# Kernel tuning notes

Measured on AMD Instinct MI355X. Metric: run time of the kernel, lower is better.

## Reference

```python
import jax, jax.numpy as jnp
import numpy as np

K_MAX = 3
ITERS = 3
NEG_BIG = -1e9


def squash(x):
    # x: [..., O]
    sn = jnp.sum(jnp.square(x), axis=-1, keepdims=True)
    factor = sn / (1.0 + sn) / jnp.sqrt(sn + 1e-8)
    return factor * x


def setup_inputs() -> dict:
    key = jax.random.key(0)
    k1, k2, k3, k4 = jax.random.split(key, 4)
    N, L, D, O = 4096, 200, 64, 64
    behavior_embs = jax.random.normal(k1, (N, L, D), dtype=jnp.float32)
    W = jax.random.normal(k2, (D, O), dtype=jnp.float32)  # init_std=1.0
    routing_logits_init = jax.random.normal(k3, (N, K_MAX, L), dtype=jnp.float32)
    seq_len = jax.random.randint(k4, (N, 1), 0, L, dtype=jnp.int32)
    return {
        "behavior_embs": behavior_embs,
        "W": W,
        "routing_logits_init": routing_logits_init,
        "seq_len": seq_len,
    }


def reference(behavior_embs, W, routing_logits_init, seq_len):
    N, L, D = behavior_embs.shape
    # mask: [N, K_MAX, L] -- valid positions along L, tiled across capsules
    mask = jnp.arange(L)[None, None, :] < seq_len[:, None, :]  # [N,1,L]
    mask = jnp.broadcast_to(mask, (N, K_MAX, L))

    mappings = jnp.matmul(behavior_embs, W)          # [N, L, O]
    m_det = jax.lax.stop_gradient(mappings)         # routing uses detached mappings

    logits = routing_logits_init                     # [N, K_MAX, L]
    for _ in range(ITERS - 1):
        padded = jnp.where(mask, logits, NEG_BIG)
        # NOTE: softmax over the capsule dim (axis=1), as in the original
        weights = jax.nn.softmax(padded, axis=1)     # [N, K_MAX, L]
        candidates = jnp.matmul(weights, m_det)      # [N, K_MAX, O]
        interests = squash(candidates)
        logits = logits + jnp.einsum('nko,nlo->nkl', interests, m_det)

    padded = jnp.where(mask, logits, NEG_BIG)
    weights = jax.nn.softmax(padded, axis=1)
    candidates = jnp.matmul(weights, mappings)       # final iter uses non-detached
    interests = squash(candidates)                   # [N, K_MAX, O]
    return interests
```

## Files before the change

kernel.cpp:

```cpp
#include <hip/hip_runtime.h>
#include <math.h>

typedef _Float16 f16;
typedef _Float16 f16x8 __attribute__((ext_vector_type(8)));
typedef float f32x4 __attribute__((ext_vector_type(4)));

#define LSEQ 200
#define LT 13
#define NCHUNK 1664
#define EBUF (NCHUNK*8)
#define SPB 4

__global__ __launch_bounds__(256, 2)
void capsule_kernel(const float* __restrict__ E,
                    const float* __restrict__ W,
                    const float* __restrict__ RL,
                    const int* __restrict__ SL,
                    float* __restrict__ out,
                    int Ntot)
{
    __shared__ __attribute__((aligned(16))) f16 e_sw[2*EBUF];
    __shared__ __attribute__((aligned(16))) f16 w_p[3*224];
    __shared__ __attribute__((aligned(16))) f16 i_c[3*80];
    __shared__ __attribute__((aligned(16))) f16 iw_c[3*72];
    __shared__ __attribute__((aligned(16))) float cand[192];

    const int n0 = blockIdx.x * SPB;
    const int t = threadIdx.x;
    const int lane = t & 63;
    const int wv = t >> 6;
    const int q = lane >> 4;
    const int cc = lane & 15;
    const int cmin = cc < 3 ? cc : 2;
    const int o_own = wv*16 + cc;

    f16x8 wB0, wB1, wt0, wt1;
    {
        f16x8 h;
        #pragma unroll
        for (int j = 0; j < 8; j++) h[j] = (f16)W[(q*8 + j)*64 + o_own];
        wB0 = h;
        #pragma unroll
        for (int j = 0; j < 8; j++) h[j] = (f16)W[(32 + q*8 + j)*64 + o_own];
        wB1 = h;
        const float4 a0 = *(const float4*)(W + o_own*64 + q*8);
        const float4 b0 = *(const float4*)(W + o_own*64 + q*8 + 4);
        f16x8 g0 = { (f16)a0.x,(f16)a0.y,(f16)a0.z,(f16)a0.w,
                     (f16)b0.x,(f16)b0.y,(f16)b0.z,(f16)b0.w };
        wt0 = g0;
        const float4 a1 = *(const float4*)(W + o_own*64 + 32 + q*8);
        const float4 b1 = *(const float4*)(W + o_own*64 + 32 + q*8 + 4);
        f16x8 g1 = { (f16)a1.x,(f16)a1.y,(f16)a1.z,(f16)a1.w,
                     (f16)b1.x,(f16)b1.y,(f16)b1.z,(f16)b1.w };
        wt1 = g1;
    }

    if (t < 12) {
        const f16x8 hz = {(f16)0.f,(f16)0.f,(f16)0.f,(f16)0.f,
                          (f16)0.f,(f16)0.f,(f16)0.f,(f16)0.f};
        *(f16x8*)&w_p[(t>>2)*224 + 192 + (t&3)*8] = hz;
    }

    const float4 f4z = make_float4(0.f, 0.f, 0.f, 0.f);
    float4 va[7], vb[7];

#define STAGE_ISSUE(NN)                                                       \
    {                                                                         \
        const float* Eb_ = E + (size_t)(NN) * (LSEQ*64);                      \
        _Pragma("unroll")                                                     \
        for (int i = 0; i < 7; i++) {                                         \
            int g = t + i*256;                                                \
            va[i] = f4z; vb[i] = f4z;                                         \
            if (g < NCHUNK) {                                                 \
                int l = (g >> 7)*16 + (g & 15);                               \
                int kb = ((g >> 6) & 1)*32 + ((g >> 4) & 3)*8;                \
                if (l < LSEQ) {                                               \
                    va[i] = *(const float4*)(Eb_ + l*64 + kb);                \
                    vb[i] = *(const float4*)(Eb_ + l*64 + kb + 4);            \
                }                                                             \
            }                                                                 \
        }                                                                     \
    }

#define STAGE_COMMIT(BASE)                                                    \
    {                                                                         \
        _Pragma("unroll")                                                     \
        for (int i = 0; i < 7; i++) {                                         \
            int g = t + i*256;                                                \
            if (g < NCHUNK) {                                                 \
                f16x8 h = { (f16)va[i].x,(f16)va[i].y,(f16)va[i].z,(f16)va[i].w,\
                            (f16)vb[i].x,(f16)vb[i].y,(f16)vb[i].z,(f16)vb[i].w };\
                *(f16x8*)&e_sw[(BASE) + g*8] = h;                             \
            }                                                                 \
        }                                                                     \
    }

    if (n0 < Ntot) {
        STAGE_ISSUE(n0)
        STAGE_COMMIT(0)
    }

    for (int j = 0; j < SPB; ++j) {
        const int nn = n0 + j;
        if (nn >= Ntot) break;
        const int cur = (j & 1) * EBUF;
        const int nxt = ((j + 1) & 1) * EBUF;
        const bool pf = (j + 1 < SPB) && (nn + 1 < Ntot);

        __syncthreads();

        float lg[4][3];
        #pragma unroll
        for (int slot = 0; slot < 4; slot++) {
            int Tn = wv + slot*4;
            if (Tn < LT && lane < 16) {
                int l = Tn*16 + lane;
                if (l < LSEQ) {
                    lg[slot][0] = RL[(size_t)nn*600 + l];
                    lg[slot][1] = RL[(size_t)nn*600 + 200 + l];
                    lg[slot][2] = RL[(size_t)nn*600 + 400 + l];
                }
            }
        }
        const int s = SL[nn];

        if (pf) STAGE_ISSUE(nn + 1)

        f16x8 mc0, mc1, mc2, mc3, mc4, mc5, mc6;

#define MM_PAIR(P, MC)                                                        \
        {                                                                     \
            f32x4 c0 = {0.f, 0.f, 0.f, 0.f};                                  \
            f32x4 c1 = {0.f, 0.f, 0.f, 0.f};                                  \
            f16x8 a00 = *(f16x8*)&e_sw[cur + (((2*(P)  )*2 + 0)*64 + lane)*8];\
            c0 = __builtin_amdgcn_mfma_f32_16x16x32_f16(a00, wB0, c0, 0,0,0); \
            f16x8 a01 = *(f16x8*)&e_sw[cur + (((2*(P)  )*2 + 1)*64 + lane)*8];\
            c0 = __builtin_amdgcn_mfma_f32_16x16x32_f16(a01, wB1, c0, 0,0,0); \
            f16x8 a10 = *(f16x8*)&e_sw[cur + (((2*(P)+1)*2 + 0)*64 + lane)*8];\
            c1 = __builtin_amdgcn_mfma_f32_16x16x32_f16(a10, wB0, c1, 0,0,0); \
            f16x8 a11 = *(f16x8*)&e_sw[cur + (((2*(P)+1)*2 + 1)*64 + lane)*8];\
            c1 = __builtin_amdgcn_mfma_f32_16x16x32_f16(a11, wB1, c1, 0,0,0); \
            f16x8 hh;                                                         \
            hh[0]=(f16)c0[0]; hh[1]=(f16)c0[1]; hh[2]=(f16)c0[2]; hh[3]=(f16)c0[3];\
            hh[4]=(f16)c1[0]; hh[5]=(f16)c1[1]; hh[6]=(f16)c1[2]; hh[7]=(f16)c1[3];\
            MC = hh;                                                          \
        }

        MM_PAIR(0, mc0)
        MM_PAIR(1, mc1)
        MM_PAIR(2, mc2)
        MM_PAIR(3, mc3)
        MM_PAIR(4, mc4)
        MM_PAIR(5, mc5)
#undef MM_PAIR
        {
            f32x4 c0 = {0.f, 0.f, 0.f, 0.f};
            f16x8 a00 = *(f16x8*)&e_sw[cur + ((12*2 + 0)*64 + lane)*8];
            c0 = __builtin_amdgcn_mfma_f32_16x16x32_f16(a00, wB0, c0, 0,0,0);
            f16x8 a01 = *(f16x8*)&e_sw[cur + ((12*2 + 1)*64 + lane)*8];
            c0 = __builtin_amdgcn_mfma_f32_16x16x32_f16(a01, wB1, c0, 0,0,0);
            f16x8 hh;
            hh[0]=(f16)c0[0]; hh[1]=(f16)c0[1]; hh[2]=(f16)c0[2]; hh[3]=(f16)c0[3];
            hh[4]=(f16)0.f;   hh[5]=(f16)0.f;   hh[6]=(f16)0.f;   hh[7]=(f16)0.f;
            mc6 = hh;
        }

        if (pf) STAGE_COMMIT(nxt)

        #pragma unroll
        for (int slot = 0; slot < 4; slot++) {
            int Tn = wv + slot*4;
            if (Tn < LT && lane < 16) {
                int l = Tn*16 + lane;
                if (l < LSEQ) {
                    float w0, w1, w2;
                    if (l < s) {
                        float l0 = lg[slot][0], l1 = lg[slot][1], l2 = lg[slot][2];
                        float mx = fmaxf(fmaxf(l0, l1), l2);
                        float e0 = expf(l0 - mx), e1 = expf(l1 - mx), e2 = expf(l2 - mx);
                        float inv = 1.f / (e0 + e1 + e2);
                        w0 = e0*inv; w1 = e1*inv; w2 = e2*inv;
                    } else {
                        w0 = w1 = w2 = (1.f/3.f);
                    }
                    int wbase = (l>>5)*32 + (((l>>2)&3)<<3) + (((l>>4)&1)<<2) + (l&3);
                    w_p[wbase]       = (f16)w0;
                    w_p[224 + wbase] = (f16)w1;
                    w_p[448 + wbase] = (f16)w2;
                }
            }
        }
        __syncthreads();

        for (int iter = 0; iter < 3; iter++) {
            f32x4 ca = {0.f, 0.f, 0.f, 0.f};
#define CAND_STEP(P, MC)                                                      \
            { f16x8 a = *(f16x8*)&w_p[cmin*224 + (P)*32 + q*8];               \
              ca = __builtin_amdgcn_mfma_f32_16x16x32_f16(a, MC, ca, 0,0,0); }
            CAND_STEP(0, mc0)
            CAND_STEP(1, mc1)
            CAND_STEP(2, mc2)
            CAND_STEP(3, mc3)
            CAND_STEP(4, mc4)
            CAND_STEP(5, mc5)
            CAND_STEP(6, mc6)
#undef CAND_STEP
            if (q == 0) {
                cand[0*64 + o_own] = ca[0];
                cand[1*64 + o_own] = ca[1];
                cand[2*64 + o_own] = ca[2];
            }
            __syncthreads();

            if (t < 192) {
                float x = cand[t];
                float sq = x*x;
                #pragma unroll
                for (int off = 32; off >= 1; off >>= 1) sq += __shfl_xor(sq, off, 64);
                float factor = sq / ((1.f + sq) * sqrtf(sq + 1e-8f));
                float y = factor * x;
                if (iter < 2) {
                    i_c[(t >> 6)*80 + (t & 63)] = (f16)y;
                } else {
                    out[(size_t)nn*192 + t] = y;
                }
            }
            if (iter == 2) break;
            __syncthreads();

            {
                f16x8 ia0 = *(f16x8*)&i_c[cmin*80 + q*8];
                f16x8 ia1 = *(f16x8*)&i_c[cmin*80 + 32 + q*8];
                f32x4 dw = {0.f, 0.f, 0.f, 0.f};
                dw = __builtin_amdgcn_mfma_f32_16x16x32_f16(ia0, wt0, dw, 0,0,0);
                dw = __builtin_amdgcn_mfma_f32_16x16x32_f16(ia1, wt1, dw, 0,0,0);
                if (q == 0) {
                    iw_c[0*72 + o_own] = (f16)dw[0];
                    iw_c[1*72 + o_own] = (f16)dw[1];
                    iw_c[2*72 + o_own] = (f16)dw[2];
                }
            }
            __syncthreads();

            f16x8 iwa0 = *(f16x8*)&iw_c[cmin*72 + q*8];
            f16x8 iwa1 = *(f16x8*)&iw_c[cmin*72 + 32 + q*8];
            #pragma unroll
            for (int slot = 0; slot < 4; slot++) {
                int Tn = wv + slot*4;
                if (Tn < LT) {
                    f32x4 da = {0.f, 0.f, 0.f, 0.f};
                    f16x8 b0 = *(f16x8*)&e_sw[cur + ((Tn*2 + 0)*64 + lane)*8];
                    da = __builtin_amdgcn_mfma_f32_16x16x32_f16(iwa0, b0, da, 0,0,0);
                    f16x8 b1 = *(f16x8*)&e_sw[cur + ((Tn*2 + 1)*64 + lane)*8];
                    da = __builtin_amdgcn_mfma_f32_16x16x32_f16(iwa1, b1, da, 0,0,0);
                    if (lane < 16) {
                        int l = Tn*16 + lane;
                        if (l < LSEQ) {
                            float w0, w1, w2;
                            if (l < s) {
                                float l0 = lg[slot][0] + da[0];
                                float l1 = lg[slot][1] + da[1];
                                float l2 = lg[slot][2] + da[2];
                                lg[slot][0] = l0; lg[slot][1] = l1; lg[slot][2] = l2;
                                float mx = fmaxf(fmaxf(l0, l1), l2);
                                float e0 = expf(l0 - mx), e1 = expf(l1 - mx), e2 = expf(l2 - mx);
                                float inv = 1.f / (e0 + e1 + e2);
                                w0 = e0*inv; w1 = e1*inv; w2 = e2*inv;
                            } else {
                                w0 = w1 = w2 = (1.f/3.f);
                            }
                            int wbase = (l>>5)*32 + (((l>>2)&3)<<3) + (((l>>4)&1)<<2) + (l&3);
                            w_p[wbase]       = (f16)w0;
                            w_p[224 + wbase] = (f16)w1;
                            w_p[448 + wbase] = (f16)w2;
                        }
                    }
                }
            }
            __syncthreads();
        }
    }
#undef STAGE_ISSUE
#undef STAGE_COMMIT
}

extern "C" void kernel_launch(void* const* d_in, const int* in_sizes, int n_in,
                              void* d_out, int out_size, void* d_ws, size_t ws_size,
                              hipStream_t stream) {
    const float* E  = (const float*)d_in[0];
    const float* W  = (const float*)d_in[1];
    const float* RL = (const float*)d_in[2];
    const int*   SL = (const int*)d_in[3];
    float* o = (float*)d_out;
    const int N = in_sizes[3];
    const int NB = (N + SPB - 1) / SPB;
    capsule_kernel<<<dim3(NB), dim3(256), 0, stream>>>(E, W, RL, SL, o, N);
}
```

Measured before the change: 311.1 us.

## Single-buffer embedding tile and raise occupancy, prefetching during routing iterations

Replaces the double-buffered fp16 embedding tile in shared memory with a single buffer, halving LDS per block, and raises the launch-bounds target from 2 to 4 blocks per CU. The prefetch of the next sample's embeddings is now issued at routing iteration 1 and written to LDS at iteration 2, once the current tile is no longer read. This trades explicit double-buffer overlap for more resident blocks to hide latency. The tighter register budget must still hold the 56 prefetch floats, which risks spills. The overlap window is also shorter.

```diff
diff --git a/kernel.cpp b/kernel.cpp
--- a/kernel.cpp
+++ b/kernel.cpp
@@ -8,10 +8,9 @@
 #define LSEQ 200
 #define LT 13
 #define NCHUNK 1664
-#define EBUF (NCHUNK*8)
 #define SPB 4
 
-__global__ __launch_bounds__(256, 2)
+__global__ __launch_bounds__(256, 4)
 void capsule_kernel(const float* __restrict__ E,
                     const float* __restrict__ W,
                     const float* __restrict__ RL,
@@ -19,7 +18,7 @@
                     float* __restrict__ out,
                     int Ntot)
 {
-    __shared__ __attribute__((aligned(16))) f16 e_sw[2*EBUF];
+    __shared__ __attribute__((aligned(16))) f16 e_sw[NCHUNK*8];
     __shared__ __attribute__((aligned(16))) f16 w_p[3*224];
     __shared__ __attribute__((aligned(16))) f16 i_c[3*80];
     __shared__ __attribute__((aligned(16))) f16 iw_c[3*72];
@@ -82,7 +81,7 @@
         }                                                                     \
     }
 
-#define STAGE_COMMIT(BASE)                                                    \
+#define STAGE_COMMIT()                                                        \
     {                                                                         \
         _Pragma("unroll")                                                     \
         for (int i = 0; i < 7; i++) {                                         \
@@ -90,24 +89,20 @@
             if (g < NCHUNK) {                                                 \
                 f16x8 h = { (f16)va[i].x,(f16)va[i].y,(f16)va[i].z,(f16)va[i].w,\
                             (f16)vb[i].x,(f16)vb[i].y,(f16)vb[i].z,(f16)vb[i].w };\
-                *(f16x8*)&e_sw[(BASE) + g*8] = h;                             \
+                *(f16x8*)&e_sw[g*8] = h;                                      \
             }                                                                 \
         }                                                                     \
     }
 
     if (n0 < Ntot) {
         STAGE_ISSUE(n0)
-        STAGE_COMMIT(0)
+        STAGE_COMMIT()
     }
 
     for (int j = 0; j < SPB; ++j) {
         const int nn = n0 + j;
         if (nn >= Ntot) break;
-        const int cur = (j & 1) * EBUF;
-        const int nxt = ((j + 1) & 1) * EBUF;
         const bool pf = (j + 1 < SPB) && (nn + 1 < Ntot);
-
-        __syncthreads();
 
         float lg[4][3];
         #pragma unroll
@@ -124,7 +119,7 @@
         }
         const int s = SL[nn];
 
-        if (pf) STAGE_ISSUE(nn + 1)
+        __syncthreads();
 
         f16x8 mc0, mc1, mc2, mc3, mc4, mc5, mc6;
 
@@ -132,13 +127,13 @@
         {                                                                     \
             f32x4 c0 = {0.f, 0.f, 0.f, 0.f};                                  \
             f32x4 c1 = {0.f, 0.f, 0.f, 0.f};                                  \
-            f16x8 a00 = *(f16x8*)&e_sw[cur + (((2*(P)  )*2 + 0)*64 + lane)*8];\
+            f16x8 a00 = *(f16x8*)&e_sw[(((2*(P)  )*2 + 0)*64 + lane)*8];      \
             c0 = __builtin_amdgcn_mfma_f32_16x16x32_f16(a00, wB0, c0, 0,0,0); \
-            f16x8 a01 = *(f16x8*)&e_sw[cur + (((2*(P)  )*2 + 1)*64 + lane)*8];\
+            f16x8 a01 = *(f16x8*)&e_sw[(((2*(P)  )*2 + 1)*64 + lane)*8];      \
             c0 = __builtin_amdgcn_mfma_f32_16x16x32_f16(a01, wB1, c0, 0,0,0); \
-            f16x8 a10 = *(f16x8*)&e_sw[cur + (((2*(P)+1)*2 + 0)*64 + lane)*8];\
+            f16x8 a10 = *(f16x8*)&e_sw[(((2*(P)+1)*2 + 0)*64 + lane)*8];      \
             c1 = __builtin_amdgcn_mfma_f32_16x16x32_f16(a10, wB0, c1, 0,0,0); \
-            f16x8 a11 = *(f16x8*)&e_sw[cur + (((2*(P)+1)*2 + 1)*64 + lane)*8];\
+            f16x8 a11 = *(f16x8*)&e_sw[(((2*(P)+1)*2 + 1)*64 + lane)*8];      \
             c1 = __builtin_amdgcn_mfma_f32_16x16x32_f16(a11, wB1, c1, 0,0,0); \
             f16x8 hh;                                                         \
             hh[0]=(f16)c0[0]; hh[1]=(f16)c0[1]; hh[2]=(f16)c0[2]; hh[3]=(f16)c0[3];\
@@ -155,17 +150,15 @@
 #undef MM_PAIR
         {
             f32x4 c0 = {0.f, 0.f, 0.f, 0.f};
-            f16x8 a00 = *(f16x8*)&e_sw[cur + ((12*2 + 0)*64 + lane)*8];
+            f16x8 a00 = *(f16x8*)&e_sw[((12*2 + 0)*64 + lane)*8];
             c0 = __builtin_amdgcn_mfma_f32_16x16x32_f16(a00, wB0, c0, 0,0,0);
-            f16x8 a01 = *(f16x8*)&e_sw[cur + ((12*2 + 1)*64 + lane)*8];
+            f16x8 a01 = *(f16x8*)&e_sw[((12*2 + 1)*64 + lane)*8];
             c0 = __builtin_amdgcn_mfma_f32_16x16x32_f16(a01, wB1, c0, 0,0,0);
             f16x8 hh;
             hh[0]=(f16)c0[0]; hh[1]=(f16)c0[1]; hh[2]=(f16)c0[2]; hh[3]=(f16)c0[3];
             hh[4]=(f16)0.f;   hh[5]=(f16)0.f;   hh[6]=(f16)0.f;   hh[7]=(f16)0.f;
             mc6 = hh;
         }
-
-        if (pf) STAGE_COMMIT(nxt)
 
         #pragma unroll
         for (int slot = 0; slot < 4; slot++) {
@@ -193,6 +186,14 @@
         __syncthreads();
 
         for (int iter = 0; iter < 3; iter++) {
+            if (iter == 1 && pf) {
+                STAGE_ISSUE(nn + 1)
+                __builtin_amdgcn_sched_barrier(0);
+            }
+            if (iter == 2 && pf) {
+                STAGE_COMMIT()
+            }
+
             f32x4 ca = {0.f, 0.f, 0.f, 0.f};
 #define CAND_STEP(P, MC)                                                      \
             { f16x8 a = *(f16x8*)&w_p[cmin*224 + (P)*32 + q*8];               \
@@ -249,9 +250,9 @@
                 int Tn = wv + slot*4;
                 if (Tn < LT) {
                     f32x4 da = {0.f, 0.f, 0.f, 0.f};
-                    f16x8 b0 = *(f16x8*)&e_sw[cur + ((Tn*2 + 0)*64 + lane)*8];
+                    f16x8 b0 = *(f16x8*)&e_sw[((Tn*2 + 0)*64 + lane)*8];
                     da = __builtin_amdgcn_mfma_f32_16x16x32_f16(iwa0, b0, da, 0,0,0);
-                    f16x8 b1 = *(f16x8*)&e_sw[cur + ((Tn*2 + 1)*64 + lane)*8];
+                    f16x8 b1 = *(f16x8*)&e_sw[((Tn*2 + 1)*64 + lane)*8];
                     da = __builtin_amdgcn_mfma_f32_16x16x32_f16(iwa1, b1, da, 0,0,0);
                     if (lane < 16) {
                         int l = Tn*16 + lane;
```

Result: slower. 393.9 us (+26.6%).
